# Performance work log

Measured on AMD Instinct MI355X. Metric: run time of the kernel, lower is better.

The kernel has to match this reference:

```python
import jax, jax.numpy as jnp
import numpy as np

WINDOW_SIZE = 2
CART_PIXEL_WIDTH = 640
CART_RESOLUTION = 0.2592


def _to_radar_frame(pix):
    # pix: [B, N, 2] pixel coords -> metric coords in radar frame
    if CART_PIXEL_WIDTH % 2 == 0:
        cmin = (CART_PIXEL_WIDTH / 2 - 0.5) * CART_RESOLUTION
    else:
        cmin = (CART_PIXEL_WIDTH // 2) * CART_RESOLUTION
    cmin = jnp.float32(cmin)
    x = pix[..., 0]
    y = pix[..., 1]
    # R = [[0,-res],[res,0]], t = [cmin, -cmin]
    return jnp.stack([cmin - CART_RESOLUTION * y,
                      CART_RESOLUTION * x - cmin], axis=-1)


def setup_inputs() -> dict:
    key = jax.random.key(0)
    k1, k2, k3 = jax.random.split(key, 3)
    B, N = 4096, 1024
    keypoint_coords = jax.random.uniform(k1, (B * WINDOW_SIZE, N, 2), jnp.float32) * CART_PIXEL_WIDTH
    tgt_coords = jax.random.uniform(k2, (B, N, 2), jnp.float32) * CART_PIXEL_WIDTH
    weights = jax.random.uniform(k3, (B, 1, N), jnp.float32, minval=0.01, maxval=1.0)
    return {"keypoint_coords": keypoint_coords, "tgt_coords": tgt_coords, "weights": weights}


def reference(keypoint_coords, tgt_coords, weights):
    # take every window_size-th frame as source
    src = keypoint_coords[::WINDOW_SIZE]                 # [B, N, 2]
    src = _to_radar_frame(src)
    tgt = _to_radar_frame(tgt_coords)
    # pad z=0 to make 3D points
    src = jnp.pad(src, ((0, 0), (0, 0), (0, 1)))         # [B, N, 3]
    tgt = jnp.pad(tgt, ((0, 0), (0, 0), (0, 1)))
    src = jnp.swapaxes(src, 1, 2)                        # [B, 3, N]
    tgt = jnp.swapaxes(tgt, 1, 2)

    w = jnp.sum(weights, axis=2, keepdims=True)          # [B, 1, 1]
    src_centroid = jnp.sum(src * weights, axis=2, keepdims=True) / w   # [B, 3, 1]
    tgt_centroid = jnp.sum(tgt * weights, axis=2, keepdims=True) / w
    src_centered = src - src_centroid
    tgt_centered = tgt - tgt_centroid

    # weighted cross-covariance: [B, 3, 3]
    W = jnp.einsum('bin,bjn->bij', tgt_centered * weights, src_centered) / w

    U, _, Vh = jnp.linalg.svd(W)
    V = jnp.swapaxes(Vh, -1, -2)
    det_UV = jnp.linalg.det(U) * jnp.linalg.det(V)       # [B]
    s = jnp.stack([jnp.ones_like(det_UV), jnp.ones_like(det_UV), det_UV], axis=-1)  # diag of S
    # R_tgt_src = U @ diag(s) @ V^T
    R_tgt_src = jnp.einsum('bij,bj,bkj->bik', U, s, V)

    # t_tgt_src_insrc = src_centroid - R^T @ tgt_centroid
    t_tgt_src_insrc = src_centroid - jnp.einsum('bji,bjk->bik', R_tgt_src, tgt_centroid)
    t_src_tgt_intgt = -jnp.einsum('bij,bjk->bik', R_tgt_src, t_tgt_src_insrc)
    return jnp.swapaxes(R_tgt_src, -1, -2), t_src_tgt_intgt
```

## Files before the change

kernel.cpp:

```cpp
#include <hip/hip_runtime.h>

#define NPTS 1024
#define RES 0.2592f
#define CMIN (319.5f * 0.2592f)

__global__ __launch_bounds__(256) void kabsch_kernel(
    const float* __restrict__ kp,
    const float* __restrict__ tg,
    const float* __restrict__ wt,
    float* __restrict__ outR,
    float* __restrict__ outT)
{
    const int b   = blockIdx.x;
    const int tid = threadIdx.x;

    const float4* wp = (const float4*)(wt + (long)b * NPTS);
    const float4* sp = (const float4*)(kp + (long)(2 * b) * NPTS * 2);
    const float4* tp = (const float4*)(tg + (long)b * NPTS * 2);

    float4 w4  = wp[tid];
    float4 s01 = sp[tid * 2];
    float4 s23 = sp[tid * 2 + 1];
    float4 t01 = tp[tid * 2];
    float4 t23 = tp[tid * 2 + 1];

    float acc[9];
#pragma unroll
    for (int i = 0; i < 9; ++i) acc[i] = 0.f;

    float pxs[4] = {s01.x, s01.z, s23.x, s23.z};
    float pys[4] = {s01.y, s01.w, s23.y, s23.w};
    float qxs[4] = {t01.x, t01.z, t23.x, t23.z};
    float qys[4] = {t01.y, t01.w, t23.y, t23.w};
    float ws[4]  = {w4.x, w4.y, w4.z, w4.w};

#pragma unroll
    for (int k = 0; k < 4; ++k) {
        float sx = CMIN - RES * pys[k];
        float sy = RES * pxs[k] - CMIN;
        float tx = CMIN - RES * qys[k];
        float ty = RES * qxs[k] - CMIN;
        float w  = ws[k];
        float wtx = w * tx;
        float wty = w * ty;
        acc[0] += w;
        acc[1] += w * sx;
        acc[2] += w * sy;
        acc[3] += wtx;
        acc[4] += wty;
        acc[5] += wtx * sx;
        acc[6] += wtx * sy;
        acc[7] += wty * sx;
        acc[8] += wty * sy;
    }

#pragma unroll
    for (int i = 0; i < 9; ++i) {
#pragma unroll
        for (int off = 32; off >= 1; off >>= 1)
            acc[i] += __shfl_xor(acc[i], off, 64);
    }

    __shared__ float red[4][9];
    const int wave = tid >> 6;
    const int lane = tid & 63;
    if (lane == 0) {
#pragma unroll
        for (int i = 0; i < 9; ++i) red[wave][i] = acc[i];
    }
    __syncthreads();

    if (tid == 0) {
        float s[9];
#pragma unroll
        for (int i = 0; i < 9; ++i)
            s[i] = red[0][i] + red[1][i] + red[2][i] + red[3][i];

        const float Sw  = s[0];
        const float Ssx = s[1], Ssy = s[2];
        const float Stx = s[3], Sty = s[4];
        const float M00 = s[5], M01 = s[6], M10 = s[7], M11 = s[8];

        const float a  = M00 * Sw - Stx * Ssx;
        const float bb = M01 * Sw - Stx * Ssy;
        const float c  = M10 * Sw - Sty * Ssx;
        const float d  = M11 * Sw - Sty * Ssy;
        const float det = a * d - bb * c;

        float Q00, Q01, Q10, Q11, sgn;
        if (det >= 0.f) {
            float p = a + d, q = c - bb;
            float h = rsqrtf(p * p + q * q);
            p *= h; q *= h;
            Q00 = p;  Q01 = -q;
            Q10 = q;  Q11 = p;
            sgn = 1.f;
        } else {
            float p = a - d, q = bb + c;
            float h = rsqrtf(p * p + q * q);
            p *= h; q *= h;
            Q00 = p;  Q01 = q;
            Q10 = q;  Q11 = -p;
            sgn = -1.f;
        }

        const float inv = 1.f / Sw;
        const float sbx = Ssx * inv, sby = Ssy * inv;
        const float tbx = Stx * inv, tby = Sty * inv;

        const float t1x = sbx - (Q00 * tbx + Q10 * tby);
        const float t1y = sby - (Q01 * tbx + Q11 * tby);
        const float t2x = -(Q00 * t1x + Q01 * t1y);
        const float t2y = -(Q10 * t1x + Q11 * t1y);

        float* r = outR + (long)b * 9;
        r[0] = Q00; r[1] = Q10; r[2] = 0.f;
        r[3] = Q01; r[4] = Q11; r[5] = 0.f;
        r[6] = 0.f; r[7] = 0.f; r[8] = sgn;

        float* t = outT + (long)b * 3;
        t[0] = t2x; t[1] = t2y; t[2] = 0.f;
    }
}

extern "C" void kernel_launch(void* const* d_in, const int* in_sizes, int n_in,
                              void* d_out, int out_size, void* d_ws, size_t ws_size,
                              hipStream_t stream) {
    const float* kp = (const float*)d_in[0];
    const float* tg = (const float*)d_in[1];
    const float* wt = (const float*)d_in[2];

    const int B = in_sizes[2] / NPTS;
    float* outR = (float*)d_out;
    float* outT = (float*)d_out + (long)B * 9;

    kabsch_kernel<<<B, 256, 0, stream>>>(kp, tg, wt, outR, outT);
}
```

Baseline: 20.65 us.

## Assign one wavefront per batch item instead of one block per item

Each 64-lane wavefront now processes a whole batch element, looping over eight chunks of points with coalesced float4/float2 loads, and each block handles four batch items. This removes the shared-memory cross-wave reduction and the __syncthreads barrier, and spreads the final 2x2 rotation solve across four lanes per block instead of one thread. The trade-off is more serial work per wave and fewer in-flight loads per point, and the launch assumes B is divisible by 4.

Result: no change. 20.38 us, median of 2 (-1.3%).

```diff
diff --git a/kernel.cpp b/kernel.cpp
--- a/kernel.cpp
+++ b/kernel.cpp
@@ -4,54 +4,56 @@
 #define RES 0.2592f
 #define CMIN (319.5f * 0.2592f)
 
-__global__ __launch_bounds__(256) void kabsch_kernel(
+__global__ __launch_bounds__(256, 4) void kabsch_kernel(
     const float* __restrict__ kp,
     const float* __restrict__ tg,
     const float* __restrict__ wt,
     float* __restrict__ outR,
     float* __restrict__ outT)
 {
-    const int b   = blockIdx.x;
-    const int tid = threadIdx.x;
+    const int wave = threadIdx.x >> 6;
+    const int lane = threadIdx.x & 63;
+    const int b    = blockIdx.x * 4 + wave;
 
-    const float4* wp = (const float4*)(wt + (long)b * NPTS);
+    const float2* wp = (const float2*)(wt + (long)b * NPTS);
     const float4* sp = (const float4*)(kp + (long)(2 * b) * NPTS * 2);
     const float4* tp = (const float4*)(tg + (long)b * NPTS * 2);
-
-    float4 w4  = wp[tid];
-    float4 s01 = sp[tid * 2];
-    float4 s23 = sp[tid * 2 + 1];
-    float4 t01 = tp[tid * 2];
-    float4 t23 = tp[tid * 2 + 1];
 
     float acc[9];
 #pragma unroll
     for (int i = 0; i < 9; ++i) acc[i] = 0.f;
 
-    float pxs[4] = {s01.x, s01.z, s23.x, s23.z};
-    float pys[4] = {s01.y, s01.w, s23.y, s23.w};
-    float qxs[4] = {t01.x, t01.z, t23.x, t23.z};
-    float qys[4] = {t01.y, t01.w, t23.y, t23.w};
-    float ws[4]  = {w4.x, w4.y, w4.z, w4.w};
+#pragma unroll
+    for (int c = 0; c < 8; ++c) {
+        const int idx = lane + 64 * c;
+        float4 s4 = sp[idx];
+        float4 t4 = tp[idx];
+        float2 w2 = wp[idx];
 
 #pragma unroll
-    for (int k = 0; k < 4; ++k) {
-        float sx = CMIN - RES * pys[k];
-        float sy = RES * pxs[k] - CMIN;
-        float tx = CMIN - RES * qys[k];
-        float ty = RES * qxs[k] - CMIN;
-        float w  = ws[k];
-        float wtx = w * tx;
-        float wty = w * ty;
-        acc[0] += w;
-        acc[1] += w * sx;
-        acc[2] += w * sy;
-        acc[3] += wtx;
-        acc[4] += wty;
-        acc[5] += wtx * sx;
-        acc[6] += wtx * sy;
-        acc[7] += wty * sx;
-        acc[8] += wty * sy;
+        for (int k = 0; k < 2; ++k) {
+            float px = k ? s4.z : s4.x;
+            float py = k ? s4.w : s4.y;
+            float qx = k ? t4.z : t4.x;
+            float qy = k ? t4.w : t4.y;
+            float w  = k ? w2.y : w2.x;
+
+            float sx = CMIN - RES * py;
+            float sy = RES * px - CMIN;
+            float tx = CMIN - RES * qy;
+            float ty = RES * qx - CMIN;
+            float wtx = w * tx;
+            float wty = w * ty;
+            acc[0] += w;
+            acc[1] += w * sx;
+            acc[2] += w * sy;
+            acc[3] += wtx;
+            acc[4] += wty;
+            acc[5] += wtx * sx;
+            acc[6] += wtx * sy;
+            acc[7] += wty * sx;
+            acc[8] += wty * sy;
+        }
     }
 
 #pragma unroll
@@ -61,25 +63,11 @@
             acc[i] += __shfl_xor(acc[i], off, 64);
     }
 
-    __shared__ float red[4][9];
-    const int wave = tid >> 6;
-    const int lane = tid & 63;
     if (lane == 0) {
-#pragma unroll
-        for (int i = 0; i < 9; ++i) red[wave][i] = acc[i];
-    }
-    __syncthreads();
-
-    if (tid == 0) {
-        float s[9];
-#pragma unroll
-        for (int i = 0; i < 9; ++i)
-            s[i] = red[0][i] + red[1][i] + red[2][i] + red[3][i];
-
-        const float Sw  = s[0];
-        const float Ssx = s[1], Ssy = s[2];
-        const float Stx = s[3], Sty = s[4];
-        const float M00 = s[5], M01 = s[6], M10 = s[7], M11 = s[8];
+        const float Sw  = acc[0];
+        const float Ssx = acc[1], Ssy = acc[2];
+        const float Stx = acc[3], Sty = acc[4];
+        const float M00 = acc[5], M01 = acc[6], M10 = acc[7], M11 = acc[8];
 
         const float a  = M00 * Sw - Stx * Ssx;
         const float bb = M01 * Sw - Stx * Ssy;
@@ -134,5 +122,5 @@
     float* outR = (float*)d_out;
     float* outT = (float*)d_out + (long)B * 9;
 
-    kabsch_kernel<<<B, 256, 0, stream>>>(kp, tg, wt, outR, outT);
+    kabsch_kernel<<<B / 4, 256, 0, stream>>>(kp, tg, wt, outR, outT);
 }
```
